# Optimization experiments

Hardware: AMD Instinct MI355X
Metric: run time of the kernel (lower is better)

Reference implementation:

```python
import jax, jax.numpy as jnp
import numpy as np

N_FFT = 1024
HOP = 512


def _overlap_add_50pct(frames):
    """Stateful 50% overlap-add. frames: (B, N, n_fft) -> (B, N, hop).
    Each frame is split into (curr, next); output[t] = curr[t] + next[t-1]."""
    xs = jnp.moveaxis(frames, 1, 0)  # (N, B, n_fft) for scan over frames

    def step(carry, x):
        x_curr = x[..., :HOP]
        x_next = x[..., HOP:]
        return x_next, x_curr + carry

    init = jnp.zeros((xs.shape[1], HOP), dtype=frames.dtype)
    _, ys = jax.lax.scan(step, init, xs)  # ys: (N, B, hop)
    return jnp.moveaxis(ys, 0, 1)  # (B, N, hop)


def _istft(re, im):
    spec = jax.lax.complex(re, im)               # (B, N, n_fft//2+1)
    frames = jnp.fft.irfft(spec, n=N_FFT, axis=-1)  # (B, N, n_fft), real IFFT
    frames = frames * jnp.asarray(0.5, frames.dtype)  # MulHalf (window_fn=None path)
    return _overlap_add_50pct(frames)            # (B, N, hop)


def setup_inputs() -> dict:
    key = jax.random.key(0)
    k1, k2 = jax.random.split(key)
    B, N = 8, 4000
    re = jax.random.normal(k1, (B, N, N_FFT // 2 + 1), dtype=jnp.float32)
    im = jax.random.normal(k2, (B, N, N_FFT // 2 + 1), dtype=jnp.float32)
    return {"re": re, "im": im}


def reference(re, im):
    return _istft(re, im)
```

## Files before the change

kernel.cpp:

```cpp
#include <hip/hip_runtime.h>
#include <math.h>

#define NBINS 513
#define NROWS 4000
#define BATCH 8
#define FPW   8
#define CHAINS_PER_BATCH (NROWS / FPW)

typedef const __attribute__((address_space(1))) void* gvp;
typedef __attribute__((address_space(3))) void* lvp;

__device__ __forceinline__ void cmul(float& ar, float& ai, float br, float bi) {
    const float t = ar * br - ai * bi;
    ai = ar * bi + ai * br;
    ar = t;
}

__device__ __forceinline__ void idft8(float* xr, float* xi) {
    const float S = 0.70710678118654752440f;
    float er[4], ei[4], orr[4], oi[4];
    #pragma unroll
    for (int j = 0; j < 4; ++j) {
        er[j]  = xr[j] + xr[j+4];  ei[j] = xi[j] + xi[j+4];
        orr[j] = xr[j] - xr[j+4];  oi[j] = xi[j] - xi[j+4];
    }
    const float f1r = S * (orr[1] - oi[1]), f1i = S * (orr[1] + oi[1]);
    const float f2r = -oi[2],               f2i = orr[2];
    const float f3r = S * (-orr[3] - oi[3]), f3i = S * (orr[3] - oi[3]);
    {
        const float eer = er[0]+er[2], eei = ei[0]+ei[2];
        const float eor = er[0]-er[2], eoi = ei[0]-ei[2];
        const float oer = er[1]+er[3], oei = ei[1]+ei[3];
        const float oor = er[1]-er[3], ooi = ei[1]-ei[3];
        xr[0] = eer + oer;  xi[0] = eei + oei;
        xr[2] = eor - ooi;  xi[2] = eoi + oor;
        xr[4] = eer - oer;  xi[4] = eei - oei;
        xr[6] = eor + ooi;  xi[6] = eoi - oor;
    }
    {
        const float eer = orr[0]+f2r, eei = oi[0]+f2i;
        const float eor = orr[0]-f2r, eoi = oi[0]-f2i;
        const float oer = f1r+f3r,    oei = f1i+f3i;
        const float oor = f1r-f3r,    ooi = f1i-f3i;
        xr[1] = eer + oer;  xi[1] = eei + oei;
        xr[3] = eor - ooi;  xi[3] = eoi + oor;
        xr[5] = eer - oer;  xi[5] = eei - oei;
        xr[7] = eor + ooi;  xi[7] = eoi - oor;
    }
}

__global__ __launch_bounds__(64) void istft_kernel(
    const float* __restrict__ re, const float* __restrict__ im,
    float* __restrict__ out)
{
    __shared__ float st[2][2][516];

    const int u  = threadIdx.x;
    const int b  = blockIdx.y;
    const int t0 = blockIdx.x * FPW;

    const int k1 = u >> 3;
    const int k2 = u & 7;

    const float w0 = 6.283185307179586476925f / 1024.0f;
    const float F  = 4.8828125e-4f;

    float2 twn[8];
    #pragma unroll
    for (int j = 0; j < 8; ++j) {
        float s, c; sincosf(w0 * (float)(u + 64 * j), &s, &c);
        twn[j] = make_float2(-F * s, F * c);
    }
    float2 wA, wB0, wBs;
    {
        float s, c;
        sincosf(w0 * (float)(16 * k1), &s, &c);     wA  = make_float2(c, s);
        sincosf(w0 * (float)(2 * k2 * k1), &s, &c); wB0 = make_float2(c, s);
        sincosf(w0 * (float)(16 * k2), &s, &c);     wBs = make_float2(c, s);
    }

    float2 cc[4];
    #pragma unroll
    for (int m = 0; m < 4; ++m) cc[m] = make_float2(0.f, 0.f);

    const float* rebase = re + (size_t)b * NROWS * NBINS;
    const float* imbase = im + (size_t)b * NROWS * NBINS;

    auto stage = [&](int t, int buf) {
        const float* rp = rebase + (size_t)t * NBINS;
        const float* ip = imbase + (size_t)t * NBINS;
        #pragma unroll
        for (int jj = 0; jj < 8; ++jj)
            __builtin_amdgcn_global_load_lds((gvp)(rp + 64 * jj + u),
                                             (lvp)&st[buf][0][64 * jj], 4, 0, 0);
        __builtin_amdgcn_global_load_lds((gvp)(rp + 449 + u),
                                         (lvp)&st[buf][0][449], 4, 0, 0);
        #pragma unroll
        for (int jj = 0; jj < 8; ++jj)
            __builtin_amdgcn_global_load_lds((gvp)(ip + 64 * jj + u),
                                             (lvp)&st[buf][1][64 * jj], 4, 0, 0);
        __builtin_amdgcn_global_load_lds((gvp)(ip + 449 + u),
                                         (lvp)&st[buf][1][449], 4, 0, 0);
    };

    if (t0 == 0) {
        #pragma unroll
        for (int j = 0; j < 8; ++j) { st[0][0][u + 64 * j] = 0.f; st[0][1][u + 64 * j] = 0.f; }
        if (u == 0) { st[0][0][512] = 0.f; st[0][1][512] = 0.f; }
    } else {
        stage(t0 - 1, 0);
    }
    asm volatile("s_waitcnt vmcnt(0)" ::: "memory");

    for (int it = 0; it <= FPW; ++it) {
        const int t = t0 - 1 + it;
        const int c = it & 1;

        if (it >= 2)      { asm volatile("s_waitcnt vmcnt(4)" ::: "memory"); }
        else if (it == 1) { asm volatile("s_waitcnt vmcnt(0)" ::: "memory"); }

        float zr8[8], zi8[8];
        {
            const float* fr = st[c][0];
            const float* fi = st[c][1];
            #pragma unroll
            for (int j = 0; j < 8; ++j) {
                const int k = u + 64 * j;
                float xr = fr[k], xi = fi[k];
                float rc = fr[512 - k], ic = -fi[512 - k];
                if (k == 0) { xi = 0.f; ic = 0.f; }
                const float er0 = xr + rc, ei0 = xi + ic;
                const float hr0 = xr - rc, hi0 = xi - ic;
                zr8[j] = F * er0 + (twn[j].x * hr0 - twn[j].y * hi0);
                zi8[j] = F * ei0 + (twn[j].x * hi0 + twn[j].y * hr0);
            }
        }

        if (it < FPW) stage(t + 1, c ^ 1);

        float2* ex2 = (float2*)&st[c][0][0];

        idft8(zr8, zi8);
        {
            float tr = wA.x, ti = wA.y;
            #pragma unroll
            for (int m0 = 1; m0 < 8; ++m0) {
                cmul(zr8[m0], zi8[m0], tr, ti);
                cmul(tr, ti, wA.x, wA.y);
            }
        }
        #pragma unroll
        for (int m0 = 0; m0 < 8; ++m0)
            ex2[64 * m0 + 8 * ((k1 ^ m0) & 7) + k2] = make_float2(zr8[m0], zi8[m0]);
        #pragma unroll
        for (int kk = 0; kk < 8; ++kk) {
            const float2 v = ex2[64 * k1 + 8 * ((kk ^ k1) & 7) + k2];
            zr8[kk] = v.x; zi8[kk] = v.y;
        }

        idft8(zr8, zi8);
        {
            float tr = wB0.x, ti = wB0.y;
            #pragma unroll
            for (int m1 = 0; m1 < 8; ++m1) {
                cmul(zr8[m1], zi8[m1], tr, ti);
                cmul(tr, ti, wBs.x, wBs.y);
            }
        }
        #pragma unroll
        for (int m1 = 0; m1 < 8; ++m1)
            ex2[64 * k2 + 8 * ((m1 ^ k2) & 7) + k1] = make_float2(zr8[m1], zi8[m1]);
        #pragma unroll
        for (int kk = 0; kk < 8; ++kk) {
            const float2 v = ex2[64 * kk + 8 * ((k1 ^ kk) & 7) + k2];
            zr8[kk] = v.x; zi8[kk] = v.y;
        }

        idft8(zr8, zi8);

        if (it >= 1) {
            float2* orow = (float2*)(out + ((size_t)b * NROWS + (size_t)t) * 512);
            #pragma unroll
            for (int m = 0; m < 4; ++m)
                orow[u + 64 * m] = make_float2(zr8[m] + cc[m].x, zi8[m] + cc[m].y);
        }
        #pragma unroll
        for (int m = 0; m < 4; ++m) cc[m] = make_float2(zr8[m + 4], zi8[m + 4]);
    }
}

extern "C" void kernel_launch(void* const* d_in, const int* in_sizes, int n_in,
                              void* d_out, int out_size, void* d_ws, size_t ws_size,
                              hipStream_t stream) {
    const float* re = (const float*)d_in[0];
    const float* im = (const float*)d_in[1];
    float* out = (float*)d_out;
    dim3 grid(CHAINS_PER_BATCH, BATCH);
    istft_kernel<<<grid, 64, 0, stream>>>(re, im, out);
}
```

Baseline: 45.82 us.

## Pack two real frames into one complex 1024-point IFFT per pass

The kernel now processes frames in pairs, packing row a as the real part and row a+1 as the imaginary part of a single full-length complex inverse FFT. This replaces the per-frame half-length complex transform with its Hermitian pre-twiddle, and reorganises the FFT as radix-16 followed by two radix-8 stages. The overlap-add is done directly from the real and imaginary outputs, with double-buffered staging of two rows at a time. The aim is fewer twiddle multiplies and fewer loop iterations per frame. In exchange it uses more registers and LDS, needs the last-row clamp and edge handling, and the wait-count logic changes.

```diff
diff --git a/kernel.cpp b/kernel.cpp
--- a/kernel.cpp
+++ b/kernel.cpp
@@ -5,6 +5,7 @@
 #define NROWS 4000
 #define BATCH 8
 #define FPW   8
+#define NPAIR 5
 #define CHAINS_PER_BATCH (NROWS / FPW)
 
 typedef const __attribute__((address_space(1))) void* gvp;
@@ -49,143 +50,208 @@
     }
 }
 
+__device__ __forceinline__ void idft16(float* xr, float* xi) {
+    float er[8], ei[8], og[8], oi[8];
+    #pragma unroll
+    for (int r = 0; r < 8; ++r) {
+        er[r] = xr[2*r];     ei[r] = xi[2*r];
+        og[r] = xr[2*r+1];   oi[r] = xi[2*r+1];
+    }
+    idft8(er, ei);
+    idft8(og, oi);
+    const float C1 = 0.92387953251128675613f;
+    const float S1 = 0.38268343236508977173f;
+    const float C2 = 0.70710678118654752440f;
+    xr[0] = er[0] + og[0];  xi[0] = ei[0] + oi[0];
+    xr[8] = er[0] - og[0];  xi[8] = ei[0] - oi[0];
+    { const float tr = C1*og[1] - S1*oi[1], ti = C1*oi[1] + S1*og[1];
+      xr[1]=er[1]+tr; xi[1]=ei[1]+ti; xr[9]=er[1]-tr;  xi[9]=ei[1]-ti; }
+    { const float tr = C2*(og[2]-oi[2]),  ti = C2*(oi[2]+og[2]);
+      xr[2]=er[2]+tr; xi[2]=ei[2]+ti; xr[10]=er[2]-tr; xi[10]=ei[2]-ti; }
+    { const float tr = S1*og[3] - C1*oi[3], ti = S1*oi[3] + C1*og[3];
+      xr[3]=er[3]+tr; xi[3]=ei[3]+ti; xr[11]=er[3]-tr; xi[11]=ei[3]-ti; }
+    { const float tr = -oi[4], ti = og[4];
+      xr[4]=er[4]+tr; xi[4]=ei[4]+ti; xr[12]=er[4]-tr; xi[12]=ei[4]-ti; }
+    { const float tr = -S1*og[5] - C1*oi[5], ti = -S1*oi[5] + C1*og[5];
+      xr[5]=er[5]+tr; xi[5]=ei[5]+ti; xr[13]=er[5]-tr; xi[13]=ei[5]-ti; }
+    { const float tr = -C2*(og[6]+oi[6]), ti = C2*(og[6]-oi[6]);
+      xr[6]=er[6]+tr; xi[6]=ei[6]+ti; xr[14]=er[6]-tr; xi[14]=ei[6]-ti; }
+    { const float tr = -C1*og[7] - S1*oi[7], ti = -C1*oi[7] + S1*og[7];
+      xr[7]=er[7]+tr; xi[7]=ei[7]+ti; xr[15]=er[7]-tr; xi[15]=ei[7]-ti; }
+}
+
 __global__ __launch_bounds__(64) void istft_kernel(
     const float* __restrict__ re, const float* __restrict__ im,
     float* __restrict__ out)
 {
-    __shared__ float st[2][2][516];
-
-    const int u  = threadIdx.x;
-    const int b  = blockIdx.y;
-    const int t0 = blockIdx.x * FPW;
-
-    const int k1 = u >> 3;
-    const int k2 = u & 7;
+    __shared__ float st[2][2][2][516];
+
+    const int u   = threadIdx.x;
+    const int b   = blockIdx.y;
+    const int t0  = blockIdx.x * FPW;
+    const int ulo = u & 7;
+    const int uhi = u >> 3;
 
     const float w0 = 6.283185307179586476925f / 1024.0f;
     const float F  = 4.8828125e-4f;
 
-    float2 twn[8];
-    #pragma unroll
-    for (int j = 0; j < 8; ++j) {
-        float s, c; sincosf(w0 * (float)(u + 64 * j), &s, &c);
-        twn[j] = make_float2(-F * s, F * c);
-    }
-    float2 wA, wB0, wBs;
+    float2 wU, wT2;
     {
         float s, c;
-        sincosf(w0 * (float)(16 * k1), &s, &c);     wA  = make_float2(c, s);
-        sincosf(w0 * (float)(2 * k2 * k1), &s, &c); wB0 = make_float2(c, s);
-        sincosf(w0 * (float)(16 * k2), &s, &c);     wBs = make_float2(c, s);
-    }
-
-    float2 cc[4];
+        sincosf(w0 * (float)u, &s, &c);          wU  = make_float2(c, s);
+        sincosf(w0 * (float)(16 * ulo), &s, &c); wT2 = make_float2(c, s);
+    }
+
+    float cc[8];
     #pragma unroll
-    for (int m = 0; m < 4; ++m) cc[m] = make_float2(0.f, 0.f);
+    for (int m = 0; m < 8; ++m) cc[m] = 0.f;
 
     const float* rebase = re + (size_t)b * NROWS * NBINS;
     const float* imbase = im + (size_t)b * NROWS * NBINS;
 
-    auto stage = [&](int t, int buf) {
+    auto stageRow = [&](int t, int pb, int rs) {
         const float* rp = rebase + (size_t)t * NBINS;
         const float* ip = imbase + (size_t)t * NBINS;
         #pragma unroll
         for (int jj = 0; jj < 8; ++jj)
             __builtin_amdgcn_global_load_lds((gvp)(rp + 64 * jj + u),
-                                             (lvp)&st[buf][0][64 * jj], 4, 0, 0);
+                                             (lvp)&st[pb][rs][0][64 * jj], 4, 0, 0);
         __builtin_amdgcn_global_load_lds((gvp)(rp + 449 + u),
-                                         (lvp)&st[buf][0][449], 4, 0, 0);
+                                         (lvp)&st[pb][rs][0][449], 4, 0, 0);
         #pragma unroll
         for (int jj = 0; jj < 8; ++jj)
             __builtin_amdgcn_global_load_lds((gvp)(ip + 64 * jj + u),
-                                             (lvp)&st[buf][1][64 * jj], 4, 0, 0);
+                                             (lvp)&st[pb][rs][1][64 * jj], 4, 0, 0);
         __builtin_amdgcn_global_load_lds((gvp)(ip + 449 + u),
-                                         (lvp)&st[buf][1][449], 4, 0, 0);
+                                         (lvp)&st[pb][rs][1][449], 4, 0, 0);
     };
 
     if (t0 == 0) {
         #pragma unroll
-        for (int j = 0; j < 8; ++j) { st[0][0][u + 64 * j] = 0.f; st[0][1][u + 64 * j] = 0.f; }
-        if (u == 0) { st[0][0][512] = 0.f; st[0][1][512] = 0.f; }
+        for (int j = 0; j < 8; ++j) {
+            st[0][0][0][u + 64 * j] = 0.f; st[0][0][1][u + 64 * j] = 0.f;
+        }
+        if (u == 0) { st[0][0][0][512] = 0.f; st[0][0][1][512] = 0.f; }
+        stageRow(0, 0, 1);
     } else {
-        stage(t0 - 1, 0);
+        stageRow(t0 - 1, 0, 0);
+        stageRow(t0,     0, 1);
     }
     asm volatile("s_waitcnt vmcnt(0)" ::: "memory");
 
-    for (int it = 0; it <= FPW; ++it) {
-        const int t = t0 - 1 + it;
-        const int c = it & 1;
-
-        if (it >= 2)      { asm volatile("s_waitcnt vmcnt(4)" ::: "memory"); }
-        else if (it == 1) { asm volatile("s_waitcnt vmcnt(0)" ::: "memory"); }
-
-        float zr8[8], zi8[8];
-        {
-            const float* fr = st[c][0];
-            const float* fi = st[c][1];
+    for (int ip = 0; ip < NPAIR; ++ip) {
+        const int a    = t0 - 1 + 2 * ip;
+        const int cbuf = ip & 1;
+
+        if (ip == 1)      { asm volatile("s_waitcnt vmcnt(8)"  ::: "memory"); }
+        else if (ip >= 2) { asm volatile("s_waitcnt vmcnt(16)" ::: "memory"); }
+
+        float zr[16], zi[16];
+        {
+            const float* ra = st[cbuf][0][0];
+            const float* ia = st[cbuf][0][1];
+            const float* rb = st[cbuf][1][0];
+            const float* ib = st[cbuf][1][1];
             #pragma unroll
             for (int j = 0; j < 8; ++j) {
                 const int k = u + 64 * j;
-                float xr = fr[k], xi = fi[k];
-                float rc = fr[512 - k], ic = -fi[512 - k];
-                if (k == 0) { xi = 0.f; ic = 0.f; }
-                const float er0 = xr + rc, ei0 = xi + ic;
-                const float hr0 = xr - rc, hi0 = xi - ic;
-                zr8[j] = F * er0 + (twn[j].x * hr0 - twn[j].y * hi0);
-                zi8[j] = F * ei0 + (twn[j].x * hi0 + twn[j].y * hr0);
-            }
-        }
-
-        if (it < FPW) stage(t + 1, c ^ 1);
-
-        float2* ex2 = (float2*)&st[c][0][0];
-
-        idft8(zr8, zi8);
-        {
-            float tr = wA.x, ti = wA.y;
-            #pragma unroll
-            for (int m0 = 1; m0 < 8; ++m0) {
-                cmul(zr8[m0], zi8[m0], tr, ti);
-                cmul(tr, ti, wA.x, wA.y);
-            }
-        }
-        #pragma unroll
-        for (int m0 = 0; m0 < 8; ++m0)
-            ex2[64 * m0 + 8 * ((k1 ^ m0) & 7) + k2] = make_float2(zr8[m0], zi8[m0]);
-        #pragma unroll
-        for (int kk = 0; kk < 8; ++kk) {
-            const float2 v = ex2[64 * k1 + 8 * ((kk ^ k1) & 7) + k2];
-            zr8[kk] = v.x; zi8[kk] = v.y;
-        }
-
-        idft8(zr8, zi8);
-        {
-            float tr = wB0.x, ti = wB0.y;
-            #pragma unroll
-            for (int m1 = 0; m1 < 8; ++m1) {
-                cmul(zr8[m1], zi8[m1], tr, ti);
-                cmul(tr, ti, wBs.x, wBs.y);
-            }
-        }
-        #pragma unroll
-        for (int m1 = 0; m1 < 8; ++m1)
-            ex2[64 * k2 + 8 * ((m1 ^ k2) & 7) + k1] = make_float2(zr8[m1], zi8[m1]);
-        #pragma unroll
-        for (int kk = 0; kk < 8; ++kk) {
-            const float2 v = ex2[64 * kk + 8 * ((k1 ^ kk) & 7) + k2];
-            zr8[kk] = v.x; zi8[kk] = v.y;
-        }
-
-        idft8(zr8, zi8);
-
-        if (it >= 1) {
-            float2* orow = (float2*)(out + ((size_t)b * NROWS + (size_t)t) * 512);
-            #pragma unroll
-            for (int m = 0; m < 4; ++m)
-                orow[u + 64 * m] = make_float2(zr8[m] + cc[m].x, zi8[m] + cc[m].y);
-        }
-        #pragma unroll
-        for (int m = 0; m < 4; ++m) cc[m] = make_float2(zr8[m + 4], zi8[m + 4]);
+                float xra = ra[k], xia = ia[k], xrb = rb[k], xib = ib[k];
+                if (j == 0) { if (u == 0) { xia = 0.f; xib = 0.f; } }
+                zr[j] = xra - xib;
+                zi[j] = xia + xrb;
+            }
+            {
+                const int   m  = (u == 0) ? 512 : (512 - u);
+                const float s0 = (u == 0) ? 0.f : 1.f;
+                zr[8] = fmaf( s0, ib[m], ra[m]);
+                zi[8] = fmaf(-s0, ia[m], rb[m]);
+            }
+            #pragma unroll
+            for (int j = 9; j < 16; ++j) {
+                const int m = 1024 - 64 * j - u;
+                zr[j] =  ra[m] + ib[m];
+                zi[j] = -ia[m] + rb[m];
+            }
+        }
+
+        if (ip < NPAIR - 1) {
+            const int na = a + 2;
+            int nb_ = a + 3; if (nb_ > NROWS - 1) nb_ = NROWS - 1;
+            stageRow(na,  cbuf ^ 1, 0);
+            stageRow(nb_, cbuf ^ 1, 1);
+        }
+
+        idft16(zr, zi);
+        {
+            float tr = F, ti = 0.f;
+            #pragma unroll
+            for (int p = 0; p < 16; ++p) {
+                cmul(zr[p], zi[p], tr, ti);
+                cmul(tr, ti, wU.x, wU.y);
+            }
+        }
+
+        float2* ex = (float2*)&st[cbuf][0][0][0];
+
+        #pragma unroll
+        for (int c = 0; c < 8; ++c)
+            #pragma unroll
+            for (int ph = 0; ph < 2; ++ph)
+                ex[512*ph + 64*c + 8*((uhi ^ c) & 7) + ulo] =
+                    make_float2(zr[c + 8*ph], zi[c + 8*ph]);
+        #pragma unroll
+        for (int k1 = 0; k1 < 8; ++k1)
+            #pragma unroll
+            for (int ph = 0; ph < 2; ++ph) {
+                const float2 v = ex[512*ph + 64*uhi + 8*((k1 ^ uhi) & 7) + ulo];
+                zr[k1 + 8*ph] = v.x; zi[k1 + 8*ph] = v.y;
+            }
+
+        idft8(zr, zi);
+        idft8(zr + 8, zi + 8);
+        {
+            float tr = wT2.x, ti = wT2.y;
+            #pragma unroll
+            for (int qa = 1; qa < 8; ++qa) {
+                cmul(zr[qa],     zi[qa],     tr, ti);
+                cmul(zr[qa + 8], zi[qa + 8], tr, ti);
+                cmul(tr, ti, wT2.x, wT2.y);
+            }
+        }
+        #pragma unroll
+        for (int qa = 0; qa < 8; ++qa)
+            #pragma unroll
+            for (int ph = 0; ph < 2; ++ph)
+                ex[512*ph + 64*qa + 8*((uhi ^ qa) & 7) + ulo] =
+                    make_float2(zr[qa + 8*ph], zi[qa + 8*ph]);
+        #pragma unroll
+        for (int r = 0; r < 8; ++r)
+            #pragma unroll
+            for (int ph = 0; ph < 2; ++ph) {
+                const float2 v = ex[512*ph + 64*uhi + 8*((ulo ^ uhi) & 7) + r];
+                zr[r + 8*ph] = v.x; zi[r + 8*ph] = v.y;
+            }
+
+        idft8(zr, zi);
+        idft8(zr + 8, zi + 8);
+
+        {
+            float* rowa = out + ((size_t)b * NROWS + a) * 512;
+            float* rowb = out + ((size_t)b * NROWS + a + 1) * 512;
+            #pragma unroll
+            for (int ph = 0; ph < 2; ++ph) {
+                const int nb0 = ulo + 16 * uhi + 8 * ph;
+                #pragma unroll
+                for (int qb = 0; qb < 4; ++qb) {
+                    const int n  = nb0 + 128 * qb;
+                    const int rI = qb + 8 * ph;
+                    const int rH = qb + 4 + 8 * ph;
+                    if (ip >= 1)         rowa[n] = zr[rI] + cc[ph * 4 + qb];
+                    if (ip < NPAIR - 1)  rowb[n] = zi[rI] + zr[rH];
+                    cc[ph * 4 + qb] = zi[rH];
+                }
+            }
+        }
     }
 }
 
```

New measurement: 46.45 us. Within noise of the previous version (+1.4%).
